# Performance work log

Hardware: AMD Instinct MI355X
Metric: run time of the kernel (lower is better)

Reference implementation:

```python
import jax, jax.numpy as jnp
import numpy as np

N_NODES = 100000
N_EDGES = 1600000
IN_F = 128
OUT_F = 64
LN_EPS = 1e-5


def setup_inputs() -> dict:
    key = jax.random.key(0)
    ks = jax.random.split(key, 8)
    stdv = 1.0 / np.sqrt(OUT_F)
    x = jax.random.normal(ks[0], (N_NODES, IN_F), dtype=jnp.float32)
    weight = jax.random.uniform(ks[1], (IN_F, OUT_F), minval=-stdv, maxval=stdv, dtype=jnp.float32)
    bias = jnp.zeros((OUT_F,), dtype=jnp.float32)
    ln_gamma = jnp.ones((OUT_F,), dtype=jnp.float32)
    ln_beta = jnp.zeros((OUT_F,), dtype=jnp.float32)
    # residual nn.Linear(in_features, out_features): weight [out, in], bias [out]
    bound = 1.0 / np.sqrt(IN_F)
    res_w = jax.random.uniform(ks[2], (OUT_F, IN_F), minval=-bound, maxval=bound, dtype=jnp.float32)
    res_b = jax.random.uniform(ks[3], (OUT_F,), minval=-bound, maxval=bound, dtype=jnp.float32)
    edge_src = jax.random.randint(ks[4], (N_EDGES,), 0, N_NODES, dtype=jnp.int64 if jax.config.jax_enable_x64 else jnp.int32)
    edge_dst = jax.random.randint(ks[5], (N_EDGES,), 0, N_NODES, dtype=jnp.int64 if jax.config.jax_enable_x64 else jnp.int32)
    edge_weight = jax.random.uniform(ks[6], (N_EDGES,), dtype=jnp.float32)
    return {
        "x": x, "weight": weight, "bias": bias,
        "ln_gamma": ln_gamma, "ln_beta": ln_beta,
        "res_w": res_w, "res_b": res_b,
        "edge_weight": edge_weight, "edge_src": edge_src, "edge_dst": edge_dst,
    }


def reference(x, weight, bias, ln_gamma, ln_beta, res_w, res_b, edge_weight, edge_src, edge_dst):
    # support = x @ W                                   [N, OUT_F]
    support = x @ weight
    # spmm: out[d] = sum_{e: dst(e)=d} w_e * support[src(e)]
    msg = support[edge_src] * edge_weight[:, None]      # [E, OUT_F]
    out = jax.ops.segment_sum(msg, edge_dst, num_segments=x.shape[0])
    # bias
    out = out + bias
    # layernorm over feature dim
    mu = jnp.mean(out, axis=-1, keepdims=True)
    var = jnp.var(out, axis=-1, keepdims=True)
    out = (out - mu) * jax.lax.rsqrt(var + LN_EPS) * ln_gamma + ln_beta
    # relu activation
    out = jax.nn.relu(out)
    # residual linear on the input
    out = out + x @ res_w.T + res_b
    return out
```

## Files before the change

### kernel.cpp

```cpp
#include <hip/hip_runtime.h>

#define N_NODES 100000
#define N_EDGES 1600000
#define IN_F 128
#define OUT_F 64
#define LN_EPS 1e-5f

#define BSHIFT 6
#define BNODES 64
#define NB ((N_NODES + BNODES - 1) >> BSHIFT)

#define CAP 2048
#define CH 2048

#define MT 64
#define NGEMM ((N_NODES + MT - 1) / MT)
#define LDA 136

#define K1_GEMM_BLOCKS 768
#define K1_PART_BLOCKS 512
#define K1_BLOCKS (K1_GEMM_BLOCKS + K1_PART_BLOCKS)
#define K1_THREADS 256
#define K1_PART_CHUNK ((N_EDGES + K1_PART_BLOCKS - 1) / K1_PART_BLOCKS)

typedef __attribute__((ext_vector_type(8))) short short8;
typedef __attribute__((ext_vector_type(4))) float f32x4;

__device__ __forceinline__ unsigned short f2bf(float f) {
  unsigned int u = __float_as_uint(f);
  unsigned int r = (u + 0x7FFFu + ((u >> 16) & 1u)) >> 16;
  return (unsigned short)r;
}
__device__ __forceinline__ float bf2f(unsigned short h) {
  return __uint_as_float((unsigned int)h << 16);
}

__global__ __launch_bounds__(K1_THREADS) void gemm_partition(
    const float* __restrict__ x, const float* __restrict__ W,
    const float* __restrict__ res_w, const float* __restrict__ res_b,
    const int* __restrict__ esrc, const int* __restrict__ edst,
    const float* __restrict__ ew, unsigned short* __restrict__ support,
    float* __restrict__ resid, int* __restrict__ gcount,
    int2* __restrict__ part) {
  __shared__ __align__(16) char smem[34816];
  const int tid = threadIdx.x;
  const int bid = blockIdx.x;

  if (bid < K1_GEMM_BLOCKS) {
    short* bt = (short*)smem;

    for (int i = tid; i < 128 * 64; i += K1_THREADS) {
      const int k = i >> 6, n = i & 63;
      bt[n * LDA + k] = (short)f2bf(W[i]);
    }
    for (int i = tid; i < 64 * 128; i += K1_THREADS) {
      const int np = i >> 7, k = i & 127;
      bt[(64 + np) * LDA + k] = (short)f2bf(res_w[i]);
    }
    __syncthreads();

    const int w = tid >> 6;
    const int lane = tid & 63;
    const int m16 = lane & 15;
    const int quad = lane >> 4;

    float rbv[8];
#pragma unroll
    for (int nt = 0; nt < 8; ++nt)
      rbv[nt] = (nt >= 4) ? res_b[nt * 16 + m16 - 64] : 0.f;

    const float4* xr = (const float4*)x;

    for (int g = bid; g < NGEMM; g += K1_GEMM_BLOCKS) {
      const size_t row0 = (size_t)g * MT;
      const size_t arow = row0 + (size_t)(w * 16 + m16);
      const bool ok = arow < N_NODES;
      const size_t abase = arow * 32 + quad * 2;

      short8 afr[4];
#pragma unroll
      for (int kt = 0; kt < 4; ++kt) {
        float4 u = make_float4(0.f, 0.f, 0.f, 0.f);
        float4 v = make_float4(0.f, 0.f, 0.f, 0.f);
        if (ok) {
          u = xr[abase + kt * 8];
          v = xr[abase + kt * 8 + 1];
        }
        short8 a;
        a[0] = (short)f2bf(u.x); a[1] = (short)f2bf(u.y);
        a[2] = (short)f2bf(u.z); a[3] = (short)f2bf(u.w);
        a[4] = (short)f2bf(v.x); a[5] = (short)f2bf(v.y);
        a[6] = (short)f2bf(v.z); a[7] = (short)f2bf(v.w);
        afr[kt] = a;
      }

#pragma unroll
      for (int nt = 0; nt < 8; ++nt) {
        f32x4 acc = {0.f, 0.f, 0.f, 0.f};
#pragma unroll
        for (int kt = 0; kt < 4; ++kt) {
          const short8 bfr =
              *(const short8*)(&bt[(nt * 16 + m16) * LDA + kt * 32 + quad * 8]);
          acc = __builtin_amdgcn_mfma_f32_16x16x32_bf16(afr[kt], bfr, acc, 0, 0, 0);
        }
        const int col = nt * 16 + m16;
#pragma unroll
        for (int r = 0; r < 4; ++r) {
          const size_t row = row0 + w * 16 + quad * 4 + r;
          if (row < N_NODES) {
            if (col < 64) support[row * OUT_F + col] = f2bf(acc[r]);
            else          resid[row * OUT_F + (col - 64)] = acc[r] + rbv[nt];
          }
        }
      }
    }
  } else {
    int* lcnt = (int*)smem;
    int* lpos = (int*)(smem + 6256);
    for (int i = tid; i < NB; i += K1_THREADS) lcnt[i] = 0;
    __syncthreads();
    const int pb = bid - K1_GEMM_BLOCKS;
    const int beg = pb * K1_PART_CHUNK;
    const int end = min(beg + K1_PART_CHUNK, N_EDGES);
    for (int i = beg + tid; i < end; i += K1_THREADS)
      atomicAdd(&lcnt[edst[i] >> BSHIFT], 1);
    __syncthreads();
    for (int i = tid; i < NB; i += K1_THREADS)
      lpos[i] = lcnt[i] ? atomicAdd(&gcount[i], lcnt[i]) : 0;
    __syncthreads();
    for (int i = beg + tid; i < end; i += K1_THREADS) {
      const int d = edst[i];
      const int b = d >> BSHIFT;
      const int p = atomicAdd(&lpos[b], 1);
      part[(size_t)b * CAP + p] =
          make_int2((esrc[i] << BSHIFT) | (d & 63), __float_as_int(ew[i]));
    }
  }
}

__global__ __launch_bounds__(512, 4) void bucket_sort_accum(
    const unsigned short* __restrict__ support, const int2* __restrict__ part,
    const int* __restrict__ gcount, const float* __restrict__ resid,
    const float* __restrict__ bias, const float* __restrict__ gamma,
    const float* __restrict__ beta, float* __restrict__ out) {
  __shared__ int2 estage[CH];
  __shared__ int2 esorted[CH];
  __shared__ int bcnt2[BNODES];
  __shared__ int bseg[BNODES];
  __shared__ int bpos[BNODES];
  const int tid = threadIdx.x;
  const int o = tid & 63;
  const int wid = tid >> 6;
  const int b = blockIdx.x;
  const int cnt = min(gcount[b], CAP);
  const size_t beg = (size_t)b * CAP;
  const size_t end = beg + cnt;

  float acc8[8];
#pragma unroll
  for (int t = 0; t < 8; ++t) acc8[t] = 0.f;

  for (size_t base = beg; base < end; base += CH) {
    const int n = (int)min((size_t)CH, end - base);
    __syncthreads();
    if (tid < BNODES) bcnt2[tid] = 0;
    __syncthreads();

    for (int i = tid; i < n; i += 512) {
      const int2 r = part[base + i];
      estage[i] = r;
      atomicAdd(&bcnt2[r.x & 63], 1);
    }
    __syncthreads();

    if (wid == 0) {
      const int v = bcnt2[o];
      int incl = v;
#pragma unroll
      for (int off = 1; off < 64; off <<= 1) {
        const int u = __shfl_up(incl, off, 64);
        if (o >= off) incl += u;
      }
      bseg[o] = incl - v;
      bpos[o] = incl - v;
    }
    __syncthreads();

    for (int i = tid; i < n; i += 512) {
      const int2 r = estage[i];
      const int p = atomicAdd(&bpos[r.x & 63], 1);
      esorted[p] = r;
    }
    __syncthreads();

#pragma unroll
    for (int t = 0; t < 8; ++t) {
      const int j = wid * 8 + t;
      const int s = bseg[j];
      const int c = bcnt2[j];
      float a = acc8[t];
      int e = 0;
      for (; e + 4 <= c; e += 4) {
        const int2 m0 = esorted[s + e + 0];
        const int2 m1 = esorted[s + e + 1];
        const int2 m2 = esorted[s + e + 2];
        const int2 m3 = esorted[s + e + 3];
        const float v0 = bf2f(support[((size_t)((unsigned)m0.x >> 6) << 6) + o]);
        const float v1 = bf2f(support[((size_t)((unsigned)m1.x >> 6) << 6) + o]);
        const float v2 = bf2f(support[((size_t)((unsigned)m2.x >> 6) << 6) + o]);
        const float v3 = bf2f(support[((size_t)((unsigned)m3.x >> 6) << 6) + o]);
        a = fmaf(v0, __int_as_float(m0.y), a);
        a = fmaf(v1, __int_as_float(m1.y), a);
        a = fmaf(v2, __int_as_float(m2.y), a);
        a = fmaf(v3, __int_as_float(m3.y), a);
      }
      for (; e < c; ++e) {
        const int2 m = esorted[s + e];
        a = fmaf(bf2f(support[((size_t)((unsigned)m.x >> 6) << 6) + o]),
                 __int_as_float(m.y), a);
      }
      acc8[t] = a;
    }
  }

  const float bi = bias[o];
  const float ga = gamma[o];
  const float be = beta[o];
#pragma unroll
  for (int t = 0; t < 8; ++t) {
    const int j = wid * 8 + t;
    const int nid = (b << BSHIFT) + j;
    if (nid < N_NODES) {
      const float v = acc8[t] + bi;
      float s = v, sq = v * v;
#pragma unroll
      for (int off = 32; off > 0; off >>= 1) {
        s += __shfl_xor(s, off, 64);
        sq += __shfl_xor(sq, off, 64);
      }
      const float mu = s * (1.f / 64.f);
      const float var = sq * (1.f / 64.f) - mu * mu;
      const float r = rsqrtf(var + LN_EPS);
      const float nrm = fmaxf((v - mu) * r * ga + be, 0.f);
      out[(size_t)nid * OUT_F + o] = nrm + resid[(size_t)nid * OUT_F + o];
    }
  }
}

extern "C" void kernel_launch(void* const* d_in, const int* in_sizes, int n_in,
                              void* d_out, int out_size, void* d_ws,
                              size_t ws_size, hipStream_t stream) {
  const float* x      = (const float*)d_in[0];
  const float* weight = (const float*)d_in[1];
  const float* bias   = (const float*)d_in[2];
  const float* gamma  = (const float*)d_in[3];
  const float* beta   = (const float*)d_in[4];
  const float* res_w  = (const float*)d_in[5];
  const float* res_b  = (const float*)d_in[6];
  const float* ew     = (const float*)d_in[7];
  const int*   esrc   = (const int*)d_in[8];
  const int*   edst   = (const int*)d_in[9];
  float* out = (float*)d_out;

  char* ws = (char*)d_ws;
  size_t off = 0;
  auto alloc = [&](size_t bytes) {
    void* p = ws + off;
    off += (bytes + 255) & ~(size_t)255;
    return p;
  };
  unsigned short* support = (unsigned short*)alloc((size_t)N_NODES * OUT_F * 2);
  float* resid   = (float*)alloc((size_t)N_NODES * OUT_F * sizeof(float));
  int2*  part    = (int2*)alloc((size_t)NB * CAP * sizeof(int2));
  int*   gcount  = (int*)alloc((size_t)NB * sizeof(int));

  hipMemsetAsync(gcount, 0, (size_t)NB * sizeof(int), stream);

  gemm_partition<<<K1_BLOCKS, K1_THREADS, 0, stream>>>(
      x, weight, res_w, res_b, esrc, edst, ew, support, resid, gcount, part);
  bucket_sort_accum<<<NB, 512, 0, stream>>>(support, part, gcount, resid,
                                            bias, gamma, beta, out);
}
```

Before: 219.7 us.

## Interleave GEMM and partition blocks and stage edge chunks in LDS

The fused first kernel now interleaves its two roles across the grid in a 3:4 pattern, so GEMM and edge-partition blocks are scheduled on the GPU at the same time instead of back to back. The number of partition blocks doubles to 1024, which shrinks each chunk enough to fit in LDS. Each partition block copies its src, dst and weight slice into shared memory during the histogram pass, so the scatter pass no longer re-reads those arrays from global memory. In exchange, partition blocks use more LDS, and more blocks contend on the global bucket-count atomics.

```diff
diff --git a/kernel.cpp b/kernel.cpp
--- a/kernel.cpp
+++ b/kernel.cpp
@@ -17,9 +17,9 @@
 #define NGEMM ((N_NODES + MT - 1) / MT)
 #define LDA 136
 
+#define K1_BLOCKS 1792
 #define K1_GEMM_BLOCKS 768
-#define K1_PART_BLOCKS 512
-#define K1_BLOCKS (K1_GEMM_BLOCKS + K1_PART_BLOCKS)
+#define K1_PART_BLOCKS 1024
 #define K1_THREADS 256
 #define K1_PART_CHUNK ((N_EDGES + K1_PART_BLOCKS - 1) / K1_PART_BLOCKS)
 
@@ -45,8 +45,10 @@
   __shared__ __align__(16) char smem[34816];
   const int tid = threadIdx.x;
   const int bid = blockIdx.x;
-
-  if (bid < K1_GEMM_BLOCKS) {
+  const int role = bid % 7;
+
+  if (role < 3) {
+    const int gb = (bid / 7) * 3 + role;
     short* bt = (short*)smem;
 
     for (int i = tid; i < 128 * 64; i += K1_THREADS) {
@@ -71,7 +73,7 @@
 
     const float4* xr = (const float4*)x;
 
-    for (int g = bid; g < NGEMM; g += K1_GEMM_BLOCKS) {
+    for (int g = gb; g < NGEMM; g += K1_GEMM_BLOCKS) {
       const size_t row0 = (size_t)g * MT;
       const size_t arow = row0 + (size_t)(w * 16 + m16);
       const bool ok = arow < N_NODES;
@@ -115,25 +117,34 @@
       }
     }
   } else {
-    int* lcnt = (int*)smem;
-    int* lpos = (int*)(smem + 6256);
+    const int pb = (bid / 7) * 4 + (role - 3);
+    int*   ssrc = (int*)smem;
+    int*   sdst = (int*)(smem + 6256);
+    float* sew  = (float*)(smem + 12512);
+    int*   lcnt = (int*)(smem + 18768);
+    int*   lpos = (int*)(smem + 25024);
     for (int i = tid; i < NB; i += K1_THREADS) lcnt[i] = 0;
     __syncthreads();
-    const int pb = bid - K1_GEMM_BLOCKS;
     const int beg = pb * K1_PART_CHUNK;
     const int end = min(beg + K1_PART_CHUNK, N_EDGES);
-    for (int i = beg + tid; i < end; i += K1_THREADS)
-      atomicAdd(&lcnt[edst[i] >> BSHIFT], 1);
+    const int n = end - beg;
+    for (int i = tid; i < n; i += K1_THREADS) {
+      const int d = edst[beg + i];
+      ssrc[i] = esrc[beg + i];
+      sdst[i] = d;
+      sew[i] = ew[beg + i];
+      atomicAdd(&lcnt[d >> BSHIFT], 1);
+    }
     __syncthreads();
     for (int i = tid; i < NB; i += K1_THREADS)
       lpos[i] = lcnt[i] ? atomicAdd(&gcount[i], lcnt[i]) : 0;
     __syncthreads();
-    for (int i = beg + tid; i < end; i += K1_THREADS) {
-      const int d = edst[i];
+    for (int i = tid; i < n; i += K1_THREADS) {
+      const int d = sdst[i];
       const int b = d >> BSHIFT;
       const int p = atomicAdd(&lpos[b], 1);
       part[(size_t)b * CAP + p] =
-          make_int2((esrc[i] << BSHIFT) | (d & 63), __float_as_int(ew[i]));
+          make_int2((ssrc[i] << BSHIFT) | (d & 63), __float_as_int(sew[i]));
     }
   }
 }
```

Measured after the change: 210.1 us. 1.05x faster.
